# Kernel tuning notes

Measured on AMD Instinct MI355X. Metric: run time of the kernel, lower is better.

The kernel has to match this reference:

```python
import jax, jax.numpy as jnp
import numpy as np

N_VIS, N_ASSOC, N_MOTOR, IN_DIM, T = 8192, 4096, 1024, 4096, 16
TAU_MEM, V_TH, TAU_ELIG = 20.0, 1.0, 500.0


def setup_inputs() -> dict:
    key = jax.random.key(0)
    ks = jax.random.split(key, 8)
    visual_input = jax.random.uniform(ks[0], (T, IN_DIM), dtype=jnp.float32)
    noise = jax.random.uniform(ks[1], (T, N_VIS), dtype=jnp.float32)  # replaces torch.rand_like
    dopamine = jax.random.normal(ks[2], (T,), dtype=jnp.float32)
    # visual_encoder: nn.Linear(4096, n_visual) default init (kaiming-uniform-ish); use small uniform
    lim = 1.0 / np.sqrt(IN_DIM)
    W_enc = jax.random.uniform(ks[3], (N_VIS, IN_DIM), minval=-lim, maxval=lim, dtype=jnp.float32)
    b_enc = jax.random.uniform(ks[4], (N_VIS,), minval=-lim, maxval=lim, dtype=jnp.float32)
    # v_to_a / a_to_m: uniform_(0.01, 0.05), no bias
    W_va = jax.random.uniform(ks[5], (N_ASSOC, N_VIS), minval=0.01, maxval=0.05, dtype=jnp.float32)
    W_am = jax.random.uniform(ks[6], (N_MOTOR, N_ASSOC), minval=0.01, maxval=0.05, dtype=jnp.float32)
    return {"visual_input": visual_input, "noise": noise, "dopamine": dopamine,
            "W_enc": W_enc, "b_enc": b_enc, "W_va": W_va, "W_am": W_am}


def reference(visual_input, noise, dopamine, W_enc, b_enc, W_va, W_am):
    decay_m = 1.0 - 1.0 / TAU_MEM
    decay_e = 1.0 - 1.0 / TAU_ELIG
    f32 = jnp.float32

    def step(carry, xs):
        vV, vA, vM, eVA, eAM, Wva, Wam = carry
        x, u, d = xs
        # visual encoding + Bernoulli spikes
        rates = jax.nn.sigmoid(x @ W_enc.T + b_enc)             # [n_visual]
        in_spk = (u < rates * 0.3).astype(f32)
        # LIF: visual layer
        vV = vV * decay_m + in_spk
        v_spk = (vV > V_TH).astype(f32)
        vV = vV * (1.0 - v_spk)
        # LIF: assoc layer
        vA = vA * decay_m + (v_spk @ Wva.T) * 0.1
        a_spk = (vA > V_TH).astype(f32)
        vA = vA * (1.0 - a_spk)
        # LIF: motor layer
        vM = vM * decay_m + (a_spk @ Wam.T) * 0.1
        m_spk = (vM > V_TH).astype(f32)
        vM = vM * (1.0 - m_spk)
        # DA-STDP eligibility traces (rank-1 updates)
        eVA = eVA * decay_e + jnp.outer(v_spk, a_spk) * 0.01    # [n_visual, n_assoc]
        eAM = eAM * decay_e + jnp.outer(a_spk, m_spk) * 0.01    # [n_assoc, n_motor]
        # conditional dopamine-gated weight update
        gate = jnp.abs(d) > 0.1
        Wva_new = jnp.clip(Wva + jnp.clip(d * eVA.T * 0.1, -0.01, 0.01), 0.0, 1.0)
        Wam_new = jnp.clip(Wam + jnp.clip(d * eAM.T * 0.1, -0.01, 0.01), 0.0, 1.0)
        Wva = jnp.where(gate, Wva_new, Wva)
        Wam = jnp.where(gate, Wam_new, Wam)
        eVA = jnp.where(gate, eVA * 0.5, eVA)
        eAM = jnp.where(gate, eAM * 0.5, eAM)
        return (vV, vA, vM, eVA, eAM, Wva, Wam), m_spk

    init = (jnp.zeros(N_VIS, f32), jnp.zeros(N_ASSOC, f32), jnp.zeros(N_MOTOR, f32),
            jnp.zeros((N_VIS, N_ASSOC), f32), jnp.zeros((N_ASSOC, N_MOTOR), f32),
            W_va, W_am)
    _, motor_spikes = jax.lax.scan(step, init, (visual_input, noise, dopamine))
    return motor_spikes  # [T, n_motor]
```

## Files before the change

kernel.cpp:

```cpp
#include <hip/hip_runtime.h>
#include <cstdint>

#define N_VIS   8192
#define N_ASSOC 4096
#define N_MOTOR 1024
#define IN_DIM  4096
#define T_STEPS 16

template<int COLS>
__global__ __launch_bounds__(512, 4) void mv_rowwave_kernel(
        const float* __restrict__ Wg, const float* __restrict__ Vg,
        float* __restrict__ S) {
    constexpr int F4PR = COLS / 4;
    constexpr int NIT  = F4PR / 64;
    __shared__ float4 vs[2][16 * 64];
    const int tid  = threadIdx.x;
    const int lane = tid & 63, wv = tid >> 6;
    const int row  = blockIdx.x * 8 + wv;
    const float4* W4 = (const float4*)Wg + (size_t)row * F4PR;
    const float4* V4 = (const float4*)Vg;

    float acc[T_STEPS];
#pragma unroll
    for (int t = 0; t < T_STEPS; ++t) acc[t] = 0.f;

    {
        int f = tid;
#pragma unroll
        for (int p = 0; p < 2; ++p, f += 512) {
            int t = f >> 6, c = f & 63;
            vs[0][f] = V4[(size_t)t * F4PR + c];
        }
    }
    float4 w = W4[lane];
    __syncthreads();

    int buf = 0;
#pragma unroll 1
    for (int it = 0; it < NIT; ++it) {
        float4 wn = w;
        if (it + 1 < NIT) {
            wn = W4[(it + 1) * 64 + lane];
            int f = tid;
#pragma unroll
            for (int p = 0; p < 2; ++p, f += 512) {
                int t = f >> 6, c = f & 63;
                vs[buf ^ 1][f] = V4[(size_t)t * F4PR + (it + 1) * 64 + c];
            }
        }
#pragma unroll
        for (int t = 0; t < T_STEPS; ++t) {
            float4 v = vs[buf][t * 64 + lane];
            acc[t] = fmaf(w.x, v.x, acc[t]);
            acc[t] = fmaf(w.y, v.y, acc[t]);
            acc[t] = fmaf(w.z, v.z, acc[t]);
            acc[t] = fmaf(w.w, v.w, acc[t]);
        }
        __syncthreads();
        w = wn; buf ^= 1;
    }

#pragma unroll
    for (int t = 0; t < T_STEPS; ++t) {
        float a = acc[t];
        for (int o = 32; o; o >>= 1) a += __shfl_down(a, o, 64);
        acc[t] = a;
    }
    if (lane == 0) {
        float4* So = (float4*)(S + (size_t)row * 16);
#pragma unroll
        for (int q = 0; q < 4; ++q)
            So[q] = make_float4(acc[q*4], acc[q*4+1], acc[q*4+2], acc[q*4+3]);
    }
}

__global__ __launch_bounds__(256) void vlif_kernel(
        const float* __restrict__ S1, const float* __restrict__ noise,
        const float* __restrict__ b, unsigned* __restrict__ vmask,
        float* __restrict__ V) {
    const int i = blockIdx.x * 256 + threadIdx.x;
    float a[T_STEPS];
#pragma unroll
    for (int t = 0; t < T_STEPS; ++t) a[t] = S1[(size_t)i * 16 + t];
    const float bb = b[i];
    float v = 0.f;
    unsigned msk = 0;
#pragma unroll
    for (int t = 0; t < T_STEPS; ++t) {
        float logit = a[t] + bb;
        float rate = 1.0f / (1.0f + expf(-logit));
        float u = noise[t * N_VIS + i];
        float ins = (u < rate * 0.3f) ? 1.0f : 0.0f;
        v = v * 0.95f + ins;
        if (v > 1.0f) { msk |= (1u << t); v = 0.f; }
    }
    vmask[i] = msk;
#pragma unroll
    for (int t = 0; t < T_STEPS; ++t)
        V[t * N_VIS + i] = (float)((msk >> t) & 1u);
}

__global__ void ktab_kernel(const float* __restrict__ dop, float* __restrict__ K) {
    __shared__ float C[256];
    __shared__ float sd[16];
    __shared__ unsigned sg[16];
    const int p = threadIdx.x;
    if (p < 16) {
        float d = dop[p];
        sd[p] = d;
        sg[p] = (fabsf(d) > 0.1f) ? 1u : 0u;
    }
    __syncthreads();
    {
        const int s = p >> 4, r = p & 15;
        float c = 0.f;
        if (s >= r) {
            c = 1.f;
            for (int u = r; u < s; ++u) {
                if (sg[u]) c *= 0.5f;
                c *= 0.998f;
            }
        }
        C[p] = c;
    }
    __syncthreads();
    {
        const int t = p >> 4, r = p & 15;
        float kk = 0.f;
        for (int s = r; s < t; ++s)
            if (sg[s]) kk += ((sd[s] * 0.1f) * 0.01f) * C[s * 16 + r];
        K[p] = kk;
    }
}

__global__ void ovl_kernel(const unsigned* __restrict__ mask, int words_per_block,
                           int* __restrict__ ovl) {
    const int p = threadIdx.x;
    const int r = p >> 4, t = p & 15;
    const unsigned* w = mask + blockIdx.x * words_per_block;
    int c = 0;
    for (int i = 0; i < words_per_block; ++i)
        c += (int)((w[i] >> r) & (w[i] >> t) & 1u);
    atomicAdd(&ovl[p], c);
}

__global__ __launch_bounds__(64) void rec_kernel(
        const float* __restrict__ base, const int* __restrict__ ovl,
        const float* __restrict__ K, unsigned* __restrict__ mask_out,
        float* __restrict__ outp, int out_stride,
        float* __restrict__ outV, int n_rows) {
    __shared__ float KO[256];
    const int tid = threadIdx.x;
    for (int p = tid; p < 256; p += 64) {
        const int t = p >> 4, r = p & 15;
        KO[p] = K[p] * (float)ovl[r * 16 + t];
    }
    __syncthreads();

    const int j = blockIdx.x * 64 + tid;
    float br[T_STEPS];
#pragma unroll
    for (int t = 0; t < T_STEPS; ++t) br[t] = base[(size_t)j * 16 + t];

    float vmem = 0.f;
    unsigned am = 0;
#pragma unroll
    for (int t = 0; t < T_STEPS; ++t) {
        float I = br[t];
        for (int r = 0; r < t; ++r)
            if ((am >> r) & 1u) I += KO[t * 16 + r];
        vmem = vmem * 0.95f + I * 0.1f;
        const bool s = vmem > 1.0f;
        if (s) { vmem = 0.f; am |= (1u << t); }
        if (outp) outp[t * out_stride + j] = s ? 1.0f : 0.0f;
    }
    mask_out[j] = am;
    if (outV) {
#pragma unroll
        for (int t = 0; t < T_STEPS; ++t)
            outV[t * n_rows + j] = (float)((am >> t) & 1u);
    }
}

extern "C" void kernel_launch(void* const* d_in, const int* in_sizes, int n_in,
                              void* d_out, int out_size, void* d_ws, size_t ws_size,
                              hipStream_t stream) {
    const float* x     = (const float*)d_in[0];
    const float* noise = (const float*)d_in[1];
    const float* dop   = (const float*)d_in[2];
    const float* W_enc = (const float*)d_in[3];
    const float* b_enc = (const float*)d_in[4];
    const float* W_va  = (const float*)d_in[5];
    const float* W_am  = (const float*)d_in[6];
    float* out = (float*)d_out;
    (void)in_sizes; (void)n_in; (void)out_size; (void)ws_size;

    char* ws = (char*)d_ws;
    size_t off = 0;
    unsigned* vmask = (unsigned*)(ws + off); off += N_VIS * 4;
    unsigned* amask = (unsigned*)(ws + off); off += N_ASSOC * 4;
    unsigned* mmask = (unsigned*)(ws + off); off += N_MOTOR * 4;
    float*    K     = (float*)(ws + off);    off += 256 * 4;
    int*      ovl_v = (int*)(ws + off);      off += 256 * 4;
    int*      ovl_a = (int*)(ws + off);      off += 256 * 4;
    float*    S1    = (float*)(ws + off);    off += (size_t)N_VIS   * 16 * 4;
    float*    S2    = (float*)(ws + off);    off += (size_t)N_ASSOC * 16 * 4;
    float*    S3    = (float*)(ws + off);    off += (size_t)N_MOTOR * 16 * 4;
    float*    Vv    = (float*)(ws + off);    off += (size_t)T_STEPS * N_VIS * 4;
    float*    Va    = (float*)(ws + off);    off += (size_t)T_STEPS * N_ASSOC * 4;

    hipMemsetAsync(ovl_v, 0, 2 * 256 * 4, stream);

    ktab_kernel<<<1, 256, 0, stream>>>(dop, K);
    mv_rowwave_kernel<IN_DIM><<<N_VIS / 8, 512, 0, stream>>>(W_enc, x, S1);
    vlif_kernel<<<N_VIS / 256, 256, 0, stream>>>(S1, noise, b_enc, vmask, Vv);
    ovl_kernel<<<32, 256, 0, stream>>>(vmask, N_VIS / 32, ovl_v);
    mv_rowwave_kernel<N_VIS><<<N_ASSOC / 8, 512, 0, stream>>>(W_va, Vv, S2);
    rec_kernel<<<N_ASSOC / 64, 64, 0, stream>>>(S2, ovl_v, K, amask, nullptr, 0, Va, N_ASSOC);
    ovl_kernel<<<16, 256, 0, stream>>>(amask, N_ASSOC / 16, ovl_a);
    mv_rowwave_kernel<N_ASSOC><<<N_MOTOR / 8, 512, 0, stream>>>(W_am, Va, S3);
    rec_kernel<<<N_MOTOR / 64, 64, 0, stream>>>(S3, ovl_a, K, mmask, out, N_MOTOR, nullptr, 0);
}
```

Baseline: 163.9 us.

## Process two rows per wave and split columns across blocks in matvec

The matvec kernel now has each wave compute two weight rows, so every shared-memory load of the spike/input vector feeds twice as many FMAs. The column dimension is split into CS segments on separate blocks, writing partial sums that rec_kernel adds together. This restores enough blocks on the smaller assoc and motor layers to fill the GPU. The ovl memset is folded into ktab_kernel to drop one API call. Costs are higher register pressure from 32 accumulators and extra partial-sum traffic.

```diff
diff --git a/kernel.cpp b/kernel.cpp
--- a/kernel.cpp
+++ b/kernel.cpp
@@ -7,22 +7,26 @@
 #define IN_DIM  4096
 #define T_STEPS 16
 
-template<int COLS>
+template<int COLS, int CS>
 __global__ __launch_bounds__(512, 4) void mv_rowwave_kernel(
         const float* __restrict__ Wg, const float* __restrict__ Vg,
-        float* __restrict__ S) {
+        float* __restrict__ Sp, int nrows) {
     constexpr int F4PR = COLS / 4;
-    constexpr int NIT  = F4PR / 64;
+    constexpr int SEG4 = F4PR / CS;
+    constexpr int NIT  = SEG4 / 64;
     __shared__ float4 vs[2][16 * 64];
     const int tid  = threadIdx.x;
     const int lane = tid & 63, wv = tid >> 6;
-    const int row  = blockIdx.x * 8 + wv;
-    const float4* W4 = (const float4*)Wg + (size_t)row * F4PR;
-    const float4* V4 = (const float4*)Vg;
-
-    float acc[T_STEPS];
-#pragma unroll
-    for (int t = 0; t < T_STEPS; ++t) acc[t] = 0.f;
+    const int rb   = blockIdx.x / CS;
+    const int sp   = blockIdx.x % CS;
+    const int j0   = rb * 16 + wv * 2;
+    const float4* W4a = (const float4*)Wg + (size_t)j0 * F4PR + (size_t)sp * SEG4;
+    const float4* W4b = W4a + F4PR;
+    const float4* V4  = (const float4*)Vg + (size_t)sp * SEG4;
+
+    float acc[2][T_STEPS];
+#pragma unroll
+    for (int t = 0; t < T_STEPS; ++t) { acc[0][t] = 0.f; acc[1][t] = 0.f; }
 
     {
         int f = tid;
@@ -32,15 +36,16 @@
             vs[0][f] = V4[(size_t)t * F4PR + c];
         }
     }
-    float4 w = W4[lane];
+    float4 wa = W4a[lane], wb = W4b[lane];
     __syncthreads();
 
     int buf = 0;
 #pragma unroll 1
     for (int it = 0; it < NIT; ++it) {
-        float4 wn = w;
+        float4 wan = wa, wbn = wb;
         if (it + 1 < NIT) {
-            wn = W4[(it + 1) * 64 + lane];
+            wan = W4a[(it + 1) * 64 + lane];
+            wbn = W4b[(it + 1) * 64 + lane];
             int f = tid;
 #pragma unroll
             for (int p = 0; p < 2; ++p, f += 512) {
@@ -51,26 +56,36 @@
 #pragma unroll
         for (int t = 0; t < T_STEPS; ++t) {
             float4 v = vs[buf][t * 64 + lane];
-            acc[t] = fmaf(w.x, v.x, acc[t]);
-            acc[t] = fmaf(w.y, v.y, acc[t]);
-            acc[t] = fmaf(w.z, v.z, acc[t]);
-            acc[t] = fmaf(w.w, v.w, acc[t]);
+            acc[0][t] = fmaf(wa.x, v.x, acc[0][t]);
+            acc[0][t] = fmaf(wa.y, v.y, acc[0][t]);
+            acc[0][t] = fmaf(wa.z, v.z, acc[0][t]);
+            acc[0][t] = fmaf(wa.w, v.w, acc[0][t]);
+            acc[1][t] = fmaf(wb.x, v.x, acc[1][t]);
+            acc[1][t] = fmaf(wb.y, v.y, acc[1][t]);
+            acc[1][t] = fmaf(wb.z, v.z, acc[1][t]);
+            acc[1][t] = fmaf(wb.w, v.w, acc[1][t]);
         }
         __syncthreads();
-        w = wn; buf ^= 1;
+        wa = wan; wb = wbn; buf ^= 1;
     }
 
 #pragma unroll
     for (int t = 0; t < T_STEPS; ++t) {
-        float a = acc[t];
-        for (int o = 32; o; o >>= 1) a += __shfl_down(a, o, 64);
-        acc[t] = a;
+        float a0 = acc[0][t], a1 = acc[1][t];
+        for (int o = 32; o; o >>= 1) {
+            a0 += __shfl_down(a0, o, 64);
+            a1 += __shfl_down(a1, o, 64);
+        }
+        acc[0][t] = a0; acc[1][t] = a1;
     }
     if (lane == 0) {
-        float4* So = (float4*)(S + (size_t)row * 16);
-#pragma unroll
-        for (int q = 0; q < 4; ++q)
-            So[q] = make_float4(acc[q*4], acc[q*4+1], acc[q*4+2], acc[q*4+3]);
+#pragma unroll
+        for (int r = 0; r < 2; ++r) {
+            float4* So = (float4*)(Sp + ((size_t)sp * nrows + j0 + r) * 16);
+#pragma unroll
+            for (int q = 0; q < 4; ++q)
+                So[q] = make_float4(acc[r][q*4], acc[r][q*4+1], acc[r][q*4+2], acc[r][q*4+3]);
+        }
     }
 }
 
@@ -100,11 +115,13 @@
         V[t * N_VIS + i] = (float)((msk >> t) & 1u);
 }
 
-__global__ void ktab_kernel(const float* __restrict__ dop, float* __restrict__ K) {
+__global__ void ktab_kernel(const float* __restrict__ dop, float* __restrict__ K,
+                            int* __restrict__ ovl_z) {
     __shared__ float C[256];
     __shared__ float sd[16];
     __shared__ unsigned sg[16];
     const int p = threadIdx.x;
+    ovl_z[p] = 0; ovl_z[p + 256] = 0;
     if (p < 16) {
         float d = dop[p];
         sd[p] = d;
@@ -148,7 +165,7 @@
         const float* __restrict__ base, const int* __restrict__ ovl,
         const float* __restrict__ K, unsigned* __restrict__ mask_out,
         float* __restrict__ outp, int out_stride,
-        float* __restrict__ outV, int n_rows) {
+        float* __restrict__ outV, int n_rows, int cs) {
     __shared__ float KO[256];
     const int tid = threadIdx.x;
     for (int p = tid; p < 256; p += 64) {
@@ -161,6 +178,11 @@
     float br[T_STEPS];
 #pragma unroll
     for (int t = 0; t < T_STEPS; ++t) br[t] = base[(size_t)j * 16 + t];
+#pragma unroll 1
+    for (int s = 1; s < cs; ++s)
+#pragma unroll
+        for (int t = 0; t < T_STEPS; ++t)
+            br[t] += base[((size_t)s * n_rows + j) * 16 + t];
 
     float vmem = 0.f;
     unsigned am = 0;
@@ -203,21 +225,19 @@
     float*    K     = (float*)(ws + off);    off += 256 * 4;
     int*      ovl_v = (int*)(ws + off);      off += 256 * 4;
     int*      ovl_a = (int*)(ws + off);      off += 256 * 4;
-    float*    S1    = (float*)(ws + off);    off += (size_t)N_VIS   * 16 * 4;
-    float*    S2    = (float*)(ws + off);    off += (size_t)N_ASSOC * 16 * 4;
-    float*    S3    = (float*)(ws + off);    off += (size_t)N_MOTOR * 16 * 4;
+    float*    S1    = (float*)(ws + off);    off += (size_t)N_VIS * 16 * 4;
+    float*    S2    = (float*)(ws + off);    off += (size_t)2 * N_ASSOC * 16 * 4;
+    float*    S3    = (float*)(ws + off);    off += (size_t)4 * N_MOTOR * 16 * 4;
     float*    Vv    = (float*)(ws + off);    off += (size_t)T_STEPS * N_VIS * 4;
     float*    Va    = (float*)(ws + off);    off += (size_t)T_STEPS * N_ASSOC * 4;
 
-    hipMemsetAsync(ovl_v, 0, 2 * 256 * 4, stream);
-
-    ktab_kernel<<<1, 256, 0, stream>>>(dop, K);
-    mv_rowwave_kernel<IN_DIM><<<N_VIS / 8, 512, 0, stream>>>(W_enc, x, S1);
+    ktab_kernel<<<1, 256, 0, stream>>>(dop, K, ovl_v);
+    mv_rowwave_kernel<IN_DIM, 1><<<N_VIS / 16, 512, 0, stream>>>(W_enc, x, S1, N_VIS);
     vlif_kernel<<<N_VIS / 256, 256, 0, stream>>>(S1, noise, b_enc, vmask, Vv);
     ovl_kernel<<<32, 256, 0, stream>>>(vmask, N_VIS / 32, ovl_v);
-    mv_rowwave_kernel<N_VIS><<<N_ASSOC / 8, 512, 0, stream>>>(W_va, Vv, S2);
-    rec_kernel<<<N_ASSOC / 64, 64, 0, stream>>>(S2, ovl_v, K, amask, nullptr, 0, Va, N_ASSOC);
+    mv_rowwave_kernel<N_VIS, 2><<<(N_ASSOC / 16) * 2, 512, 0, stream>>>(W_va, Vv, S2, N_ASSOC);
+    rec_kernel<<<N_ASSOC / 64, 64, 0, stream>>>(S2, ovl_v, K, amask, nullptr, 0, Va, N_ASSOC, 2);
     ovl_kernel<<<16, 256, 0, stream>>>(amask, N_ASSOC / 16, ovl_a);
-    mv_rowwave_kernel<N_ASSOC><<<N_MOTOR / 8, 512, 0, stream>>>(W_am, Va, S3);
-    rec_kernel<<<N_MOTOR / 64, 64, 0, stream>>>(S3, ovl_a, K, mmask, out, N_MOTOR, nullptr, 0);
-}
+    mv_rowwave_kernel<N_ASSOC, 4><<<(N_MOTOR / 16) * 4, 512, 0, stream>>>(W_am, Va, S3, N_MOTOR);
+    rec_kernel<<<N_MOTOR / 64, 64, 0, stream>>>(S3, ovl_a, K, mmask, out, N_MOTOR, nullptr, 0, 4);
+}
```

Result: faster. 145.3 us (-11.3%).
